# Optimization experiments

Hardware: AMD Instinct MI355X
Metric: run time of the kernel (lower is better)

The kernel has to match this reference:

```python
import jax, jax.numpy as jnp
import numpy as np

N_LAYER = 4
N_HEAD = 16
N_EMBD = 1024
BLOCK = 1024
VOCAB = 100
TRANS = 16          # obs_dim + action_dim + 2 = 11 + 3 + 2
OBS_DIM = 11
ACT_DIM = 3
B, T = 2, 1024
VTOT = VOCAB * TRANS + 1  # token embedding rows
LN_EPS = 1e-5


def _layernorm(x, w, b):
    mu = jnp.mean(x, axis=-1, keepdims=True)
    var = jnp.var(x, axis=-1, keepdims=True)
    return (x - mu) * jax.lax.rsqrt(var + LN_EPS) * w + b


def _build_mask(t):
    # causal tril with every (joined_dim-1 mod joined_dim) column zeroed
    jd = OBS_DIM + ACT_DIM + 2  # 16
    m = jnp.tril(jnp.ones((t, t), dtype=bool))
    cols = jnp.arange(t)
    m = m & ((cols % jd) != (jd - 1))[None, :]
    return m  # [T, T] bool, True = keep


def setup_inputs() -> dict:
    key = jax.random.key(0)
    ks = jax.random.split(key, 24)
    C, L, F4 = N_EMBD, N_LAYER, 4 * N_EMBD
    g = lambda k, s: jax.random.normal(k, s, dtype=jnp.float32) * 0.02
    return {
        "tokens": jax.random.randint(ks[0], (B, T), 0, VTOT),
        "tok_emb": g(ks[1], (VTOT, C)),
        "pos_emb": g(ks[2], (1, BLOCK, C)),
        "Wq": g(ks[3], (L, C, C)), "bq": jnp.zeros((L, C), jnp.float32),
        "Wk": g(ks[4], (L, C, C)), "bk": jnp.zeros((L, C), jnp.float32),
        "Wv": g(ks[5], (L, C, C)), "bv": jnp.zeros((L, C), jnp.float32),
        "Wp": g(ks[6], (L, C, C)), "bp": jnp.zeros((L, C), jnp.float32),
        "ln1w": jnp.ones((L, C), jnp.float32), "ln1b": jnp.zeros((L, C), jnp.float32),
        "ln2w": jnp.ones((L, C), jnp.float32), "ln2b": jnp.zeros((L, C), jnp.float32),
        "W1": g(ks[7], (L, C, F4)), "b1": jnp.zeros((L, F4), jnp.float32),
        "W2": g(ks[8], (L, F4, C)), "b2": jnp.zeros((L, C), jnp.float32),
        "lnfw": jnp.ones((C,), jnp.float32), "lnfb": jnp.zeros((C,), jnp.float32),
        "head_w": g(ks[9], (TRANS, VOCAB + 1, C)),
    }


def _forward(tokens, tok_emb, pos_emb, Wq, bq, Wk, bk, Wv, bv, Wp, bp,
             ln1w, ln1b, ln2w, ln2b, W1, b1, W2, b2, lnfw, lnfb, head_w):
    b, t = tokens.shape
    C, H = N_EMBD, N_HEAD
    D = C // H
    scale = 1.0 / np.sqrt(D)
    mask = _build_mask(t)[None, None]  # [1,1,T,T]

    x = tok_emb[tokens] + pos_emb[:, :t, :]  # [B,T,C]
    for i in range(N_LAYER):
        h = _layernorm(x, ln1w[i], ln1b[i])
        q = (h @ Wq[i] + bq[i]).reshape(b, t, H, D).transpose(0, 2, 1, 3)
        k = (h @ Wk[i] + bk[i]).reshape(b, t, H, D).transpose(0, 2, 1, 3)
        v = (h @ Wv[i] + bv[i]).reshape(b, t, H, D).transpose(0, 2, 1, 3)
        att = jnp.einsum('bhtd,bhsd->bhts', q, k) * scale  # attn_bias=None => +0
        att = jnp.where(mask, att, -jnp.inf)
        att = jax.nn.softmax(att, axis=-1)
        y = jnp.einsum('bhts,bhsd->bhtd', att, v)
        y = y.transpose(0, 2, 1, 3).reshape(b, t, C)
        x = x + (y @ Wp[i] + bp[i])
        h2 = _layernorm(x, ln2w[i], ln2b[i])
        x = x + (jax.nn.gelu(h2 @ W1[i] + b1[i], approximate=False) @ W2[i] + b2[i])

    x = _layernorm(x, lnfw, lnfb)
    # pad_to_full_observation + EinLinear head
    n_pad = (TRANS - t % TRANS) % TRANS
    if n_pad:
        x = jnp.concatenate([x, jnp.zeros((b, n_pad, C), x.dtype)], axis=1)
    x_pad = x.reshape(-1, TRANS, C)                    # [b*n_states, TRANS, C]
    logits = jnp.einsum('eoi,bei->beo', head_w, x_pad)  # EinLinear, bias=False
    logits = logits.reshape(b, t + n_pad, VOCAB + 1)[:, :t]
    return logits


def reference(tokens, tok_emb, pos_emb, Wq, bq, Wk, bk, Wv, bv, Wp, bp,
              ln1w, ln1b, ln2w, ln2b, W1, b1, W2, b2, lnfw, lnfb, head_w):
    return _forward(tokens, tok_emb, pos_emb, Wq, bq, Wk, bk, Wv, bv, Wp, bp,
                    ln1w, ln1b, ln2w, ln2b, W1, b1, W2, b2, lnfw, lnfb, head_w)
```

## Files before the change

kernel.cpp:

```cpp
#include <hip/hip_runtime.h>
#include <hip/hip_bf16.h>
#include <math.h>

typedef unsigned short u16;
typedef __attribute__((ext_vector_type(8))) short short8;
typedef __attribute__((ext_vector_type(4))) short short4v;
typedef __attribute__((ext_vector_type(4))) float f32x4;

#define CDIM 1024
#define TDIM 1024
#define NROWS 2048
#define HEADS 16
#define HD 64
#define F4 4096

__device__ __forceinline__ u16 f2bf(float f) {
    union { float f; unsigned u; } v; v.f = f;
    unsigned r = v.u + 0x7fffu + ((v.u >> 16) & 1u);
    return (u16)(r >> 16);
}
__device__ __forceinline__ float bf2f(u16 h) {
    union { unsigned u; float f; } v; v.u = (unsigned)h << 16; return v.f;
}

__device__ __forceinline__ void gload_lds16(const void* g, void* lds) {
    __builtin_amdgcn_global_load_lds(
        (const __attribute__((address_space(1))) unsigned int*)g,
        (__attribute__((address_space(3))) unsigned int*)lds,
        16, 0, 0);
}

__device__ __forceinline__ void tile_map(int& bx, int& by, int& bz)
{
    const int gx = gridDim.x, gy = gridDim.y;
    const int fid = blockIdx.x + gx * (blockIdx.y + gy * blockIdx.z);
    const int nwg = gx * gy * gridDim.z;
    const int q = nwg >> 3, r = nwg & 7;
    const int xcd = fid & 7, t = fid >> 3;
    const int n = ((xcd < r) ? xcd * (q + 1) : r * (q + 1) + (xcd - r) * q) + t;
    const int nxy = gx * gy;
    bz = n / nxy;
    const int xy = n - bz * nxy;
    const int per_group = gx << 3;
    const int grp = xy / per_group;
    const int in = xy - grp * per_group;
    const int y0 = grp << 3;
    const int rem = gy - y0;
    const int gh = rem < 8 ? rem : 8;
    by = y0 + (in % gh);
    bx = in / gh;
}

__global__ __launch_bounds__(256)
void embed_k(const int* __restrict__ tok, const float* __restrict__ te,
             const float* __restrict__ pe, float* __restrict__ X)
{
    const int row = blockIdx.x;
    const int t = row & (TDIM - 1);
    const int tk = tok[row];
    const int c = threadIdx.x * 4;
    float4 a = *reinterpret_cast<const float4*>(te + (size_t)tk * CDIM + c);
    float4 b = *reinterpret_cast<const float4*>(pe + (size_t)t * CDIM + c);
    a.x += b.x; a.y += b.y; a.z += b.z; a.w += b.w;
    *reinterpret_cast<float4*>(X + (size_t)row * CDIM + c) = a;
}

template<bool BF16OUT>
__global__ __launch_bounds__(256)
void ln_k(const float* __restrict__ X, const float* __restrict__ g,
          const float* __restrict__ be, void* __restrict__ outp)
{
    __shared__ float red[4], red2[4];
    const int row = blockIdx.x, tid = threadIdx.x;
    const float* xr = X + (size_t)row * CDIM;
    const int c = tid * 4;
    float4 xv = *reinterpret_cast<const float4*>(xr + c);
    float s  = xv.x + xv.y + xv.z + xv.w;
    float s2 = xv.x*xv.x + xv.y*xv.y + xv.z*xv.z + xv.w*xv.w;
    #pragma unroll
    for (int off = 32; off; off >>= 1) {
        s  += __shfl_xor(s, off);
        s2 += __shfl_xor(s2, off);
    }
    if ((tid & 63) == 0) { red[tid >> 6] = s; red2[tid >> 6] = s2; }
    __syncthreads();
    const float ts  = red[0] + red[1] + red[2] + red[3];
    const float ts2 = red2[0] + red2[1] + red2[2] + red2[3];
    const float mu  = ts * (1.0f / CDIM);
    const float var = ts2 * (1.0f / CDIM) - mu * mu;
    const float rs  = rsqrtf(var + 1e-5f);
    float4 gv = *reinterpret_cast<const float4*>(g + c);
    float4 bv = *reinterpret_cast<const float4*>(be + c);
    float o0 = (xv.x - mu) * rs * gv.x + bv.x;
    float o1 = (xv.y - mu) * rs * gv.y + bv.y;
    float o2 = (xv.z - mu) * rs * gv.z + bv.z;
    float o3 = (xv.w - mu) * rs * gv.w + bv.w;
    if (BF16OUT) {
        u16 tmp[4] = { f2bf(o0), f2bf(o1), f2bf(o2), f2bf(o3) };
        u16* o = (u16*)outp + (size_t)row * CDIM + c;
        *reinterpret_cast<uint2*>(o) = *reinterpret_cast<const uint2*>(tmp);
    } else {
        float4 ov = { o0, o1, o2, o3 };
        *reinterpret_cast<float4*>((float*)outp + (size_t)row * CDIM + c) = ov;
    }
}

template<int MODE, int NZ>
__global__ __launch_bounds__(256)
void ln_red_k(float* __restrict__ X, const float* __restrict__ P,
              const float* __restrict__ g, const float* __restrict__ be,
              void* __restrict__ outp)
{
    __shared__ float red[4], red2[4];
    const int row = blockIdx.x, tid = threadIdx.x;
    const int c = tid * 4;
    float4 xv = *reinterpret_cast<const float4*>(X + (size_t)row * CDIM + c);
    #pragma unroll
    for (int z = 0; z < NZ; ++z) {
        float4 pv = *reinterpret_cast<const float4*>(P + ((size_t)z * NROWS + row) * CDIM + c);
        xv.x += pv.x; xv.y += pv.y; xv.z += pv.z; xv.w += pv.w;
    }
    if (MODE != 2)
        *reinterpret_cast<float4*>(X + (size_t)row * CDIM + c) = xv;
    float s  = xv.x + xv.y + xv.z + xv.w;
    float s2 = xv.x*xv.x + xv.y*xv.y + xv.z*xv.z + xv.w*xv.w;
    #pragma unroll
    for (int off = 32; off; off >>= 1) {
        s  += __shfl_xor(s, off);
        s2 += __shfl_xor(s2, off);
    }
    if ((tid & 63) == 0) { red[tid >> 6] = s; red2[tid >> 6] = s2; }
    __syncthreads();
    const float ts  = red[0] + red[1] + red[2] + red[3];
    const float ts2 = red2[0] + red2[1] + red2[2] + red2[3];
    const float mu  = ts * (1.0f / CDIM);
    const float var = ts2 * (1.0f / CDIM) - mu * mu;
    const float rs  = rsqrtf(var + 1e-5f);
    float4 gv = *reinterpret_cast<const float4*>(g + c);
    float4 bv = *reinterpret_cast<const float4*>(be + c);
    float o0 = (xv.x - mu) * rs * gv.x + bv.x;
    float o1 = (xv.y - mu) * rs * gv.y + bv.y;
    float o2 = (xv.z - mu) * rs * gv.z + bv.z;
    float o3 = (xv.w - mu) * rs * gv.w + bv.w;
    if (MODE == 0) {
        u16 tmp[4] = { f2bf(o0), f2bf(o1), f2bf(o2), f2bf(o3) };
        u16* o = (u16*)outp + (size_t)row * CDIM + c;
        *reinterpret_cast<uint2*>(o) = *reinterpret_cast<const uint2*>(tmp);
    } else {
        u16 hi[4] = { f2bf(o0), f2bf(o1), f2bf(o2), f2bf(o3) };
        u16 lo[4] = { f2bf(o0 - bf2f(hi[0])), f2bf(o1 - bf2f(hi[1])),
                      f2bf(o2 - bf2f(hi[2])), f2bf(o3 - bf2f(hi[3])) };
        const int b = row >> 10, p = row & 1023;
        const int e = p & 15, slot = p >> 4;
        u16* ar = (u16*)outp + (size_t)(e * 128 + b * 64 + slot) * 3072;
        *reinterpret_cast<uint2*>(ar + c)        = *reinterpret_cast<const uint2*>(hi);
        *reinterpret_cast<uint2*>(ar + 1024 + c) = *reinterpret_cast<const uint2*>(lo);
        *reinterpret_cast<uint2*>(ar + 2048 + c) = *reinterpret_cast<const uint2*>(hi);
    }
}

__global__ __launch_bounds__(256)
void convTL_k(const float* __restrict__ W, u16* __restrict__ Wt,
              const int K, const int N)
{
    __shared__ u16 s[64][72];
    const int l = blockIdx.z;
    const float* Wl = W + (size_t)l * K * N;
    u16* dst = Wt + (size_t)l * K * N;
    const int k0 = blockIdx.y * 64, n0 = blockIdx.x * 64;
    const int tr = threadIdx.x >> 4, tc = (threadIdx.x & 15) * 4;
    #pragma unroll
    for (int i = 0; i < 4; ++i) {
        int r = tr + i * 16;
        float4 w = *reinterpret_cast<const float4*>(Wl + (size_t)(k0 + r) * N + n0 + tc);
        s[r][tc + 0] = f2bf(w.x); s[r][tc + 1] = f2bf(w.y);
        s[r][tc + 2] = f2bf(w.z); s[r][tc + 3] = f2bf(w.w);
    }
    __syncthreads();
    #pragma unroll
    for (int i = 0; i < 4; ++i) {
        int n = tr + i * 16;
        u16 tmp[4];
        #pragma unroll
        for (int e = 0; e < 4; ++e) tmp[e] = s[tc + e][n];
        *reinterpret_cast<uint2*>(dst + (size_t)(n0 + n) * K + k0 + tc) =
            *reinterpret_cast<const uint2*>(tmp);
    }
}

__global__ __launch_bounds__(256)
void convT3L_k(const float* __restrict__ Wq, const float* __restrict__ Wk,
               const float* __restrict__ Wv, u16* __restrict__ Wt)
{
    __shared__ u16 s[64][72];
    const int l = blockIdx.z / 3, w = blockIdx.z % 3;
    const float* W = (w == 0 ? Wq : w == 1 ? Wk : Wv) + (size_t)l * CDIM * CDIM;
    u16* dst = Wt + (size_t)blockIdx.z * CDIM * CDIM;
    const int k0 = blockIdx.y * 64, n0 = blockIdx.x * 64;
    const int tr = threadIdx.x >> 4, tc = (threadIdx.x & 15) * 4;
    #pragma unroll
    for (int i = 0; i < 4; ++i) {
        int r = tr + i * 16;
        float4 wv4 = *reinterpret_cast<const float4*>(W + (size_t)(k0 + r) * CDIM + n0 + tc);
        s[r][tc + 0] = f2bf(wv4.x); s[r][tc + 1] = f2bf(wv4.y);
        s[r][tc + 2] = f2bf(wv4.z); s[r][tc + 3] = f2bf(wv4.w);
    }
    __syncthreads();
    #pragma unroll
    for (int i = 0; i < 4; ++i) {
        int n = tr + i * 16;
        u16 tmp[4];
        #pragma unroll
        for (int e = 0; e < 4; ++e) tmp[e] = s[tc + e][n];
        *reinterpret_cast<uint2*>(dst + (size_t)(n0 + n) * CDIM + k0 + tc) =
            *reinterpret_cast<const uint2*>(tmp);
    }
}

__global__ __launch_bounds__(256)
void conv_head_k(const float* __restrict__ HW, u16* __restrict__ Wt)
{
    const int o = blockIdx.x, e = blockIdx.y;
    const int c = threadIdx.x * 4;
    u16 hi[4] = {0, 0, 0, 0}, lo[4] = {0, 0, 0, 0};
    if (o < 101) {
        float4 w = *reinterpret_cast<const float4*>(HW + ((size_t)e * 101 + o) * 1024 + c);
        hi[0] = f2bf(w.x); hi[1] = f2bf(w.y); hi[2] = f2bf(w.z); hi[3] = f2bf(w.w);
        lo[0] = f2bf(w.x - bf2f(hi[0])); lo[1] = f2bf(w.y - bf2f(hi[1]));
        lo[2] = f2bf(w.z - bf2f(hi[2])); lo[3] = f2bf(w.w - bf2f(hi[3]));
    }
    u16* wr = Wt + (size_t)(e * 128 + o) * 3072;
    *reinterpret_cast<uint2*>(wr + c)        = *reinterpret_cast<const uint2*>(hi);
    *reinterpret_cast<uint2*>(wr + 1024 + c) = *reinterpret_cast<const uint2*>(hi);
    *reinterpret_cast<uint2*>(wr + 2048 + c) = *reinterpret_cast<const uint2*>(lo);
}

__global__ __launch_bounds__(256)
void pack_bias_all_k(const float* __restrict__ a, const float* __restrict__ b,
                     const float* __restrict__ c, float* __restrict__ o)
{
    const int l = blockIdx.x / 3, w = blockIdx.x % 3;
    const int i = threadIdx.x * 4;
    const float* s = (w == 0 ? a : w == 1 ? b : c) + (size_t)l * 1024;
    *reinterpret_cast<float4*>(o + (size_t)blockIdx.x * 1024 + i) =
        *reinterpret_cast<const float4*>(s + i);
}

template<int EPI>
__global__ __launch_bounds__(256, 2)
void gemm_bt(const u16* __restrict__ A, const u16* __restrict__ Bt,
             const float* __restrict__ bias, u16* __restrict__ outb,
             float* __restrict__ resid, u16* __restrict__ vtout,
             const int N, const int K, const int KCH)
{
    __shared__ __align__(16) u16 sA[2][2][128 * 32];
    __shared__ __align__(16) u16 sB[2][2][128 * 32];
    const int tid = threadIdx.x;
    const int lane = tid & 63, wv = tid >> 6;
    int bx, by, bz;
    tile_map(bx, by, bz);
    const int m0 = by * 128, n0 = bx * 128;
    const int kbeg = bz * KCH, kend = bz * KCH + KCH;
    const int fr = lane & 15, fq = lane >> 4;
    const int wm = wv & 1, wn = wv >> 1;
    const int srow = lane >> 2;
    const int schunk = (((lane & 3) ^ ((lane >> 3) & 3)) * 8);
    const int csw = (fr >> 1) & 3;
    const u16* Bt2 = (EPI == 3) ? Bt + (size_t)by * 128 * K : Bt;
    f32x4 acc[4][4] = {};

    float bias_r[4];
    #pragma unroll
    for (int nj = 0; nj < 4; ++nj) {
        const int col = n0 + wn * 64 + nj * 16 + fr;
        bias_r[nj] = (EPI == 3) ? 0.0f
                     : (EPI == 2 && bz != 0) ? 0.0f : bias[col];
    }

    auto stage = [&](int k0, int buf) {
        #pragma unroll
        for (int kk = 0; kk < 2; ++kk)
            #pragma unroll
            for (int i = 0; i < 2; ++i) {
                const int reg = i * 4 + wv;
                gload_lds16(A  + (size_t)(m0 + reg * 16 + srow) * K + k0 + kk * 32 + schunk,
                            &sA[buf][kk][reg * 512]);
                gload_lds16(Bt2 + (size_t)(n0 + reg * 16 + srow) * K + k0 + kk * 32 + schunk,
                            &sB[buf][kk][reg * 512]);
            }
    };

    asm volatile("s_waitcnt vmcnt(0)" ::: "memory");
    stage(kbeg, 0);
    int cur = 0;
    for (int k0 = kbeg; k0 < kend; k0 += 64) {
        asm volatile("s_waitcnt lgkmcnt(0)" ::: "memory");
        __builtin_amdgcn_s_barrier();
        if (k0 + 64 < kend) {
            stage(k0 + 64, cur ^ 1);
            asm volatile("s_waitcnt vmcnt(8)" ::: "memory");
        } else {
            asm volatile("s_waitcnt vmcnt(0)" ::: "memory");
        }
        __builtin_amdgcn_s_barrier();
        __builtin_amdgcn_s_setprio(1);
        #pragma unroll
        for (int kk = 0; kk < 2; ++kk) {
            short8 af[4], bf[4];
            #pragma unroll
            for (int mi = 0; mi < 4; ++mi)
                af[mi] = *reinterpret_cast<const short8*>(
                    &sA[cur][kk][(wm * 64 + mi * 16 + fr) * 32 + (fq ^ csw) * 8]);
            #pragma unroll
            for (int nj = 0; nj < 4; ++nj)
                bf[nj] = *reinterpret_cast<const short8*>(
                    &sB[cur][kk][(wn * 64 + nj * 16 + fr) * 32 + (fq ^ csw) * 8]);
            #pragma unroll
            for (int mi = 0; mi < 4; ++mi)
                #pragma unroll
                for (int nj = 0; nj < 4; ++nj)
                    acc[mi][nj] = __builtin_amdgcn_mfma_f32_16x16x32_bf16(af[mi], bf[nj], acc[mi][nj], 0, 0, 0);
        }
        __builtin_amdgcn_s_setprio(0);
        cur ^= 1;
    }

    #pragma unroll
    for (int nj = 0; nj < 4; ++nj) {
        const int col = n0 + wn * 64 + nj * 16 + fr;
        const float bias_v = bias_r[nj];
        #pragma unroll
        for (int mi = 0; mi < 4; ++mi) {
            const int rowb = m0 + wm * 64 + mi * 16 + fq * 4;
            if (EPI == 0 && vtout != nullptr && col >= 2048) {
                const int bidx = rowb >> 10, t = rowb & 1023, hd = col - 2048;
                u16 t4[4];
                #pragma unroll
                for (int r = 0; r < 4; ++r) t4[r] = f2bf(acc[mi][nj][r] + bias_v);
                *reinterpret_cast<uint2*>(
                    vtout + ((size_t)(bidx * 16 + (hd >> 6)) * 64 + (hd & 63)) * 1024 + t) =
                    *reinterpret_cast<const uint2*>(t4);
            } else {
                #pragma unroll
                for (int r = 0; r < 4; ++r) {
                    const int row = rowb + r;
                    float cv = acc[mi][nj][r] + bias_v;
                    if (EPI == 0) {
                        outb[(size_t)row * N + col] = f2bf(cv);
                    } else if (EPI == 1) {
                        float gl = 0.5f * cv * (1.0f + erff(cv * 0.70710678118654752f));
                        outb[(size_t)row * N + col] = f2bf(gl);
                    } else if (EPI == 2) {
                        resid[((size_t)bz * NROWS + row) * N + col] = cv;
                    } else {
                        resid[((size_t)bz * NROWS + row) * 128 + col] = cv;
                    }
                }
            }
        }
    }
}

__global__ __launch_bounds__(128)
void head_red_k(const float* __restrict__ P, float* __restrict__ out)
{
    const int pr = blockIdx.x;
    const int col = threadIdx.x;
    const int e = pr >> 7, rem = pr & 127, b = rem >> 6, slot = rem & 63;
    float s = 0.0f;
    #pragma unroll
    for (int z = 0; z < 16; ++z)
        s += P[((size_t)z * NROWS + pr) * 128 + col];
    if (col < 101)
        out[((size_t)(b << 10) + (slot << 4) + e) * 101 + col] = s;
}

__global__ __launch_bounds__(256, 4)
void attn_k(const u16* __restrict__ QKV, const u16* __restrict__ VT,
            float* __restrict__ po, float* __restrict__ plsum)
{
    __shared__ __align__(16) u16 sK[2][64][72];
    __shared__ __align__(16) u16 sV[2][64][72];
    const int tid = threadIdx.x, lane = tid & 63, wv = tid >> 6;
    const int fr = lane & 15, fq = lane >> 4;
    int bx, by, bz;
    tile_map(bx, by, bz);
    const int qt = bx, h = by, b = bz >> 2, sc = bz & 3;
    const int q0 = qt * 64;
    const int nt = qt + 1;
    const int stbeg = (nt * sc) >> 2, stend = (nt * (sc + 1)) >> 2;
    const u16* Qb = QKV + (size_t)b * TDIM * 3072 + h * HD;
    const u16* Vb = VT + ((size_t)(b * HEADS + h) * HD) * TDIM;
    const int r0 = tid >> 3, c0 = (tid & 7) * 8;

    const u16* qp = Qb + (size_t)(q0 + wv * 16 + fr) * 3072 + fq * 8;
    short8 aQ0 = *reinterpret_cast<const short8*>(qp);
    short8 aQ1 = *reinterpret_cast<const short8*>(qp + 32);

    f32x4 o[4] = {};
    float lsum = 0.0f;
    int cur = 0;

    if (stbeg < stend) {
        #pragma unroll
        for (int i = 0; i < 2; ++i) {
            const int r = r0 + i * 32;
            *reinterpret_cast<uint4*>(&sK[0][r][c0]) =
                *reinterpret_cast<const uint4*>(Qb + 1024 + (size_t)(stbeg * 64 + r) * 3072 + c0);
            *reinterpret_cast<uint4*>(&sV[0][r][c0]) =
                *reinterpret_cast<const uint4*>(Vb + (size_t)r * TDIM + stbeg * 64 + c0);
        }
        __syncthreads();
    }

    for (int st = stbeg; st < stend; ++st) {
        const int s0 = st * 64;
        const bool pf = (st + 1) < stend;
        uint4 pk[2], pv[2];
        if (pf) {
            #pragma unroll
            for (int i = 0; i < 2; ++i) {
                const int r = r0 + i * 32;
                pk[i] = *reinterpret_cast<const uint4*>(Qb + 1024 + (size_t)(s0 + 64 + r) * 3072 + c0);
                pv[i] = *reinterpret_cast<const uint4*>(Vb + (size_t)r * TDIM + s0 + 64 + c0);
            }
        }
        f32x4 sacc[4] = {};
        #pragma unroll
        for (int j = 0; j < 4; ++j) {
            short8 k0f = *reinterpret_cast<const short8*>(&sK[cur][j * 16 + fr][fq * 8]);
            sacc[j] = __builtin_amdgcn_mfma_f32_16x16x32_bf16(k0f, aQ0, sacc[j], 0, 0, 0);
            short8 k1f = *reinterpret_cast<const short8*>(&sK[cur][j * 16 + fr][32 + fq * 8]);
            sacc[j] = __builtin_amdgcn_mfma_f32_16x16x32_bf16(k1f, aQ1, sacc[j], 0, 0, 0);
        }
        const int qrow = q0 + wv * 16 + fr;
        u16 pb[4][4];
        #pragma unroll
        for (int j = 0; j < 4; ++j)
            #pragma unroll
            for (int r = 0; r < 4; ++r) {
                const int scol = s0 + j * 16 + fq * 4 + r;
                const bool keep = (scol <= qrow) && ((scol & 15) != 15);
                const float p = keep ? __expf(sacc[j][r] * 0.125f) : 0.0f;
                const u16 hb = f2bf(p);
                pb[j][r] = hb;
                lsum += bf2f(hb);
            }
        union { unsigned u[4]; short8 v; } a0, a1;
        a0.u[0] = (unsigned)pb[0][0] | ((unsigned)pb[0][1] << 16);
        a0.u[1] = (unsigned)pb[0][2] | ((unsigned)pb[0][3] << 16);
        a0.u[2] = (unsigned)pb[1][0] | ((unsigned)pb[1][1] << 16);
        a0.u[3] = (unsigned)pb[1][2] | ((unsigned)pb[1][3] << 16);
        a1.u[0] = (unsigned)pb[2][0] | ((unsigned)pb[2][1] << 16);
        a1.u[1] = (unsigned)pb[2][2] | ((unsigned)pb[2][3] << 16);
        a1.u[2] = (unsigned)pb[3][0] | ((unsigned)pb[3][1] << 16);
        a1.u[3] = (unsigned)pb[3][2] | ((unsigned)pb[3][3] << 16);
        #pragma unroll
        for (int j = 0; j < 4; ++j) {
            const u16* vrow = &sV[cur][j * 16 + fr][0];
            short4v v0 = *reinterpret_cast<const short4v*>(vrow + fq * 4);
            short4v v1 = *reinterpret_cast<const short4v*>(vrow + 16 + fq * 4);
            short8 bV0 = __builtin_shufflevector(v0, v1, 0, 1, 2, 3, 4, 5, 6, 7);
            o[j] = __builtin_amdgcn_mfma_f32_16x16x32_bf16(a0.v, bV0, o[j], 0, 0, 0);
            short4v v2 = *reinterpret_cast<const short4v*>(vrow + 32 + fq * 4);
            short4v v3 = *reinterpret_cast<const short4v*>(vrow + 48 + fq * 4);
            short8 bV1 = __builtin_shufflevector(v2, v3, 0, 1, 2, 3, 4, 5, 6, 7);
            o[j] = __builtin_amdgcn_mfma_f32_16x16x32_bf16(a1.v, bV1, o[j], 0, 0, 0);
        }
        if (pf) {
            #pragma unroll
            for (int i = 0; i < 2; ++i) {
                const int r = r0 + i * 32;
                *reinterpret_cast<uint4*>(&sK[cur ^ 1][r][c0]) = pk[i];
                *reinterpret_cast<uint4*>(&sV[cur ^ 1][r][c0]) = pv[i];
            }
            __syncthreads();
            cur ^= 1;
        }
    }

    lsum += __shfl_xor(lsum, 16);
    lsum += __shfl_xor(lsum, 32);

    const int tl = (bz * 16 + h) * 16 + qt;
    float* pt = po + (size_t)tl * 4096;
    #pragma unroll
    for (int j = 0; j < 4; ++j)
        #pragma unroll
        for (int r = 0; r < 4; ++r)
            pt[(wv * 16 + fq * 4 + r) * 64 + j * 16 + fr] = o[j][r];
    if (fq == 0) plsum[(size_t)tl * 64 + wv * 16 + fr] = lsum;
}

__global__ __launch_bounds__(256)
void attn_comb_k(const float* __restrict__ po, const float* __restrict__ plsum,
                 u16* __restrict__ Y)
{
    const int qt = blockIdx.x, h = blockIdx.y, b = blockIdx.z;
    int t[4];
    #pragma unroll
    for (int i = 0; i < 4; ++i) t[i] = ((b * 4 + i) * 16 + h) * 16 + qt;
    #pragma unroll
    for (int i = 0; i < 4; ++i) {
        const int f4 = threadIdx.x + i * 256;
        const int q = f4 >> 4, d4 = (f4 & 15) * 4;
        float4 a = *reinterpret_cast<const float4*>(po + (size_t)t[0] * 4096 + f4 * 4);
        float ls = plsum[(size_t)t[0] * 64 + q];
        #pragma unroll
        for (int k = 1; k < 4; ++k) {
            float4 c = *reinterpret_cast<const float4*>(po + (size_t)t[k] * 4096 + f4 * 4);
            a.x += c.x; a.y += c.y; a.z += c.z; a.w += c.w;
            ls += plsum[(size_t)t[k] * 64 + q];
        }
        const float rl = 1.0f / ls;
        u16 t4[4] = { f2bf(a.x * rl), f2bf(a.y * rl),
                      f2bf(a.z * rl), f2bf(a.w * rl) };
        *reinterpret_cast<uint2*>(
            Y + ((size_t)(b * TDIM + qt * 64 + q)) * CDIM + h * HD + d4) =
            *reinterpret_cast<const uint2*>(t4);
    }
}

extern "C" void kernel_launch(void* const* d_in, const int* in_sizes, int n_in,
                              void* d_out, int out_size, void* d_ws, size_t ws_size,
                              hipStream_t stream)
{
    const int*   tokens = (const int*)  d_in[0];
    const float* tok_emb= (const float*)d_in[1];
    const float* pos_emb= (const float*)d_in[2];
    const float* Wq = (const float*)d_in[3];
    const float* bq = (const float*)d_in[4];
    const float* Wk = (const float*)d_in[5];
    const float* bk = (const float*)d_in[6];
    const float* Wv = (const float*)d_in[7];
    const float* bv = (const float*)d_in[8];
    const float* Wp = (const float*)d_in[9];
    const float* bp = (const float*)d_in[10];
    const float* ln1w = (const float*)d_in[11];
    const float* ln1b = (const float*)d_in[12];
    const float* ln2w = (const float*)d_in[13];
    const float* ln2b = (const float*)d_in[14];
    const float* W1 = (const float*)d_in[15];
    const float* b1 = (const float*)d_in[16];
    const float* W2 = (const float*)d_in[17];
    const float* b2 = (const float*)d_in[18];
    const float* lnfw = (const float*)d_in[19];
    const float* lnfb = (const float*)d_in[20];
    const float* head_w = (const float*)d_in[21];
    float* out = (float*)d_out;

    char* ws = (char*)d_ws;
    float* x     = (float*)(ws);
    float* hpart = (float*)(ws);
    u16*   hbuf  = (u16*)  (ws + (8u   << 20));
    u16*   yb    = (u16*)  (ws + (8u   << 20));
    u16*   qkv   = (u16*)  (ws + (12u  << 20));
    u16*   mid   = (u16*)  (ws + (12u  << 20));
    u16*   xg    = (u16*)  (ws + (16u  << 20));
    u16*   vt    = (u16*)  (ws + (24u  << 20));
    u16*   wq_all= (u16*)  (ws + (28u  << 20));
    u16*   wp_all= (u16*)  (ws + (52u  << 20));
    u16*   w1_all= (u16*)  (ws + (60u  << 20));
    u16*   w2_all= (u16*)  (ws + (92u  << 20));
    u16*   whp   = (u16*)  (ws + (124u << 20));
    float* pbuf  = (float*)(ws + (136u << 20));
    float* po    = (float*)(ws + (136u << 20));
    float* plsum = (float*)(ws + (168u << 20));
    float* bbuf  = (float*)(ws + (169u << 20));

    embed_k<<<NROWS, 256, 0, stream>>>(tokens, tok_emb, pos_emb, x);

    convT3L_k<<<dim3(16, 16, 12), 256, 0, stream>>>(Wq, Wk, Wv, wq_all);
    convTL_k<<<dim3(16, 16, 4), 256, 0, stream>>>(Wp, wp_all, CDIM, CDIM);
    convTL_k<<<dim3(64, 16, 4), 256, 0, stream>>>(W1, w1_all, CDIM, F4);
    convTL_k<<<dim3(16, 64, 4), 256, 0, stream>>>(W2, w2_all, F4, CDIM);
    pack_bias_all_k<<<12, 256, 0, stream>>>(bq, bk, bv, bbuf);
    conv_head_k<<<dim3(128, 16), 256, 0, stream>>>(head_w, whp);

    for (int l = 0; l < 4; ++l) {
        if (l == 0)
            ln_k<true><<<NROWS, 256, 0, stream>>>(x, ln1w, ln1b, hbuf);
        else
            ln_red_k<0, 4><<<NROWS, 256, 0, stream>>>(x, pbuf, ln1w + l * CDIM, ln1b + l * CDIM, hbuf);
        gemm_bt<0><<<dim3(24, 16, 1), 256, 0, stream>>>(hbuf, wq_all + (size_t)l * 3 * CDIM * CDIM,
                                                        bbuf + (size_t)l * 3072, qkv, nullptr, vt, 3072, CDIM, CDIM);
        attn_k<<<dim3(16, HEADS, 8), 256, 0, stream>>>(qkv, vt, po, plsum);
        attn_comb_k<<<dim3(16, HEADS, 2), 256, 0, stream>>>(po, plsum, yb);

        gemm_bt<2><<<dim3(8, 16, 2), 256, 0, stream>>>(yb, wp_all + (size_t)l * CDIM * CDIM,
                                                       bp + l * CDIM, nullptr, pbuf, nullptr, CDIM, CDIM, 512);

        ln_red_k<0, 2><<<NROWS, 256, 0, stream>>>(x, pbuf, ln2w + l * CDIM, ln2b + l * CDIM, hbuf);
        gemm_bt<1><<<dim3(32, 16, 1), 256, 0, stream>>>(hbuf, w1_all + (size_t)l * CDIM * F4,
                                                        b1 + l * F4, mid, nullptr, nullptr, F4, CDIM, CDIM);
        gemm_bt<2><<<dim3(8, 16, 4), 256, 0, stream>>>(mid, w2_all + (size_t)l * CDIM * F4,
                                                       b2 + l * CDIM, nullptr, pbuf, nullptr, CDIM, F4, CDIM);
    }

    ln_red_k<2, 4><<<NROWS, 256, 0, stream>>>(x, pbuf, lnfw, lnfb, xg);
    gemm_bt<3><<<dim3(1, 16, 16), 256, 0, stream>>>(xg, whp, nullptr, nullptr, hpart, nullptr, 128, 3072, 192);
    head_red_k<<<NROWS, 128, 0, stream>>>(hpart, out);
}
```

Baseline: 928.5 us.

## Add wide 128x256 GEMM tile with 512 threads for MLP GEMMs

Adds a WIDE template variant of the bf16 GEMM that uses 512 threads (8 waves) and a 128x256 output tile, doubling the B-tile in LDS, and uses it for the two MLP GEMMs. Each A tile is reused across twice as many output columns, which cuts global A traffic and the block count. The load staging and vmcnt wait are adjusted to match. The risk is halving the grid (256 and 256 blocks), which lowers occupancy and wave-count balance on the CUs, and the LDS use per block grows.

```diff
diff --git a/kernel.cpp b/kernel.cpp
--- a/kernel.cpp
+++ b/kernel.cpp
@@ -246,20 +246,21 @@
         *reinterpret_cast<const float4*>(s + i);
 }
 
-template<int EPI>
-__global__ __launch_bounds__(256, 2)
+template<int EPI, bool WIDE>
+__global__ __launch_bounds__(WIDE ? 512 : 256, 2)
 void gemm_bt(const u16* __restrict__ A, const u16* __restrict__ Bt,
              const float* __restrict__ bias, u16* __restrict__ outb,
              float* __restrict__ resid, u16* __restrict__ vtout,
              const int N, const int K, const int KCH)
 {
+    constexpr int TN = WIDE ? 256 : 128;
     __shared__ __align__(16) u16 sA[2][2][128 * 32];
-    __shared__ __align__(16) u16 sB[2][2][128 * 32];
+    __shared__ __align__(16) u16 sB[2][2][TN * 32];
     const int tid = threadIdx.x;
     const int lane = tid & 63, wv = tid >> 6;
     int bx, by, bz;
     tile_map(bx, by, bz);
-    const int m0 = by * 128, n0 = bx * 128;
+    const int m0 = by * 128, n0 = bx * TN;
     const int kbeg = bz * KCH, kend = bz * KCH + KCH;
     const int fr = lane & 15, fq = lane >> 4;
     const int wm = wv & 1, wn = wv >> 1;
@@ -279,15 +280,27 @@
 
     auto stage = [&](int k0, int buf) {
         #pragma unroll
-        for (int kk = 0; kk < 2; ++kk)
-            #pragma unroll
-            for (int i = 0; i < 2; ++i) {
-                const int reg = i * 4 + wv;
-                gload_lds16(A  + (size_t)(m0 + reg * 16 + srow) * K + k0 + kk * 32 + schunk,
-                            &sA[buf][kk][reg * 512]);
-                gload_lds16(Bt2 + (size_t)(n0 + reg * 16 + srow) * K + k0 + kk * 32 + schunk,
-                            &sB[buf][kk][reg * 512]);
+        for (int kk = 0; kk < 2; ++kk) {
+            if constexpr (WIDE) {
+                gload_lds16(A + (size_t)(m0 + wv * 16 + srow) * K + k0 + kk * 32 + schunk,
+                            &sA[buf][kk][wv * 512]);
+                #pragma unroll
+                for (int i = 0; i < 2; ++i) {
+                    const int reg = i * 8 + wv;
+                    gload_lds16(Bt2 + (size_t)(n0 + reg * 16 + srow) * K + k0 + kk * 32 + schunk,
+                                &sB[buf][kk][reg * 512]);
+                }
+            } else {
+                #pragma unroll
+                for (int i = 0; i < 2; ++i) {
+                    const int reg = i * 4 + wv;
+                    gload_lds16(A  + (size_t)(m0 + reg * 16 + srow) * K + k0 + kk * 32 + schunk,
+                                &sA[buf][kk][reg * 512]);
+                    gload_lds16(Bt2 + (size_t)(n0 + reg * 16 + srow) * K + k0 + kk * 32 + schunk,
+                                &sB[buf][kk][reg * 512]);
+                }
             }
+        }
     };
 
     asm volatile("s_waitcnt vmcnt(0)" ::: "memory");
@@ -298,7 +311,10 @@
         __builtin_amdgcn_s_barrier();
         if (k0 + 64 < kend) {
             stage(k0 + 64, cur ^ 1);
-            asm volatile("s_waitcnt vmcnt(8)" ::: "memory");
+            if constexpr (WIDE)
+                asm volatile("s_waitcnt vmcnt(6)" ::: "memory");
+            else
+                asm volatile("s_waitcnt vmcnt(8)" ::: "memory");
         } else {
             asm volatile("s_waitcnt vmcnt(0)" ::: "memory");
         }
@@ -582,22 +598,22 @@
             ln_k<true><<<NROWS, 256, 0, stream>>>(x, ln1w, ln1b, hbuf);
         else
             ln_red_k<0, 4><<<NROWS, 256, 0, stream>>>(x, pbuf, ln1w + l * CDIM, ln1b + l * CDIM, hbuf);
-        gemm_bt<0><<<dim3(24, 16, 1), 256, 0, stream>>>(hbuf, wq_all + (size_t)l * 3 * CDIM * CDIM,
+        gemm_bt<0, false><<<dim3(24, 16, 1), 256, 0, stream>>>(hbuf, wq_all + (size_t)l * 3 * CDIM * CDIM,
                                                         bbuf + (size_t)l * 3072, qkv, nullptr, vt, 3072, CDIM, CDIM);
         attn_k<<<dim3(16, HEADS, 8), 256, 0, stream>>>(qkv, vt, po, plsum);
         attn_comb_k<<<dim3(16, HEADS, 2), 256, 0, stream>>>(po, plsum, yb);
 
-        gemm_bt<2><<<dim3(8, 16, 2), 256, 0, stream>>>(yb, wp_all + (size_t)l * CDIM * CDIM,
+        gemm_bt<2, false><<<dim3(8, 16, 2), 256, 0, stream>>>(yb, wp_all + (size_t)l * CDIM * CDIM,
                                                        bp + l * CDIM, nullptr, pbuf, nullptr, CDIM, CDIM, 512);
 
         ln_red_k<0, 2><<<NROWS, 256, 0, stream>>>(x, pbuf, ln2w + l * CDIM, ln2b + l * CDIM, hbuf);
-        gemm_bt<1><<<dim3(32, 16, 1), 256, 0, stream>>>(hbuf, w1_all + (size_t)l * CDIM * F4,
+        gemm_bt<1, true><<<dim3(16, 16, 1), 512, 0, stream>>>(hbuf, w1_all + (size_t)l * CDIM * F4,
                                                         b1 + l * F4, mid, nullptr, nullptr, F4, CDIM, CDIM);
-        gemm_bt<2><<<dim3(8, 16, 4), 256, 0, stream>>>(mid, w2_all + (size_t)l * CDIM * F4,
+        gemm_bt<2, true><<<dim3(4, 16, 4), 512, 0, stream>>>(mid, w2_all + (size_t)l * CDIM * F4,
                                                        b2 + l * CDIM, nullptr, pbuf, nullptr, CDIM, F4, CDIM);
     }
 
     ln_red_k<2, 4><<<NROWS, 256, 0, stream>>>(x, pbuf, lnfw, lnfb, xg);
-    gemm_bt<3><<<dim3(1, 16, 16), 256, 0, stream>>>(xg, whp, nullptr, nullptr, hpart, nullptr, 128, 3072, 192);
+    gemm_bt<3, false><<<dim3(1, 16, 16), 256, 0, stream>>>(xg, whp, nullptr, nullptr, hpart, nullptr, 128, 3072, 192);
     head_red_k<<<NROWS, 128, 0, stream>>>(hpart, out);
 }
```

Result: slower. 957.5 us (+3.1%).
